# Kernel optimization log

Hardware: AMD Instinct MI355X
Metric: run time of the kernel (lower is better)

Reference implementation:

```python
import jax, jax.numpy as jnp
import numpy as np

N_NODES = 100000
N_EDGES = 1600000
D_IN = 128
LAYER_SIZES = [128, 128, 64]


def setup_inputs() -> dict:
    key = jax.random.key(0)
    ks = jax.random.split(key, 12)
    x = jax.random.normal(ks[0], (N_NODES, D_IN), dtype=jnp.float32)
    edge_index = jax.random.randint(ks[1], (2, N_EDGES), 0, N_NODES, dtype=jnp.int64)
    edge_weight = jax.random.uniform(ks[2], (N_EDGES,), dtype=jnp.float32)
    inp = {"x": x, "edge_index": edge_index, "edge_weight": edge_weight}
    dims = [D_IN] + LAYER_SIZES
    for i in range(len(LAYER_SIZES)):
        fan_in, fan_out = dims[i], dims[i + 1]
        # glorot-style init like PyG GCNConv
        scale = jnp.sqrt(6.0 / (fan_in + fan_out)).astype(jnp.float32)
        inp[f"W{i}"] = jax.random.uniform(ks[3 + 2 * i], (fan_in, fan_out), dtype=jnp.float32, minval=-scale, maxval=scale)
        inp[f"b{i}"] = jnp.zeros((fan_out,), dtype=jnp.float32)
    return inp


def _gcn_norm(edge_index, edge_weight, num_nodes):
    # PyG gcn_norm with add_self_loops=True (fill value 1.0)
    src, dst = edge_index[0], edge_index[1]
    loop = jnp.arange(num_nodes, dtype=edge_index.dtype)
    src_full = jnp.concatenate([src, loop])
    dst_full = jnp.concatenate([dst, loop])
    w_full = jnp.concatenate([edge_weight, jnp.ones((num_nodes,), dtype=edge_weight.dtype)])
    deg = jax.ops.segment_sum(w_full, dst_full, num_segments=num_nodes)  # [N]
    deg_inv_sqrt = jnp.where(deg > 0, jax.lax.rsqrt(jnp.where(deg > 0, deg, 1.0)), 0.0)
    norm = deg_inv_sqrt[src_full] * w_full * deg_inv_sqrt[dst_full]  # [E+N]
    return src_full, dst_full, norm


def _gcn_conv(x, src, dst, norm, W, b):
    h = x @ W                                  # [N, d_out] dense transform
    msg = h[src] * norm[:, None]               # [E+N, d_out] gather + scale
    out = jax.ops.segment_sum(msg, dst, num_segments=x.shape[0])  # scatter-add
    return out + b


def reference(x, edge_index, edge_weight, W0, b0, W1, b1, W2, b2):
    N = x.shape[0]
    src, dst, norm = _gcn_norm(edge_index, edge_weight, N)
    x = jax.nn.relu(_gcn_conv(x, src, dst, norm, W0, b0))
    x = jax.nn.relu(_gcn_conv(x, src, dst, norm, W1, b1))
    x = _gcn_conv(x, src, dst, norm, W2, b2)  # no ReLU on final layer
    return x
```

## Files before the change

### kernel.cpp

```cpp
#include <hip/hip_runtime.h>
#include <hip/hip_fp16.h>


typedef __attribute__((ext_vector_type(8))) _Float16 f16x8;
typedef __attribute__((ext_vector_type(4))) float f32x4;

#define WQ_BITS 15
#define WQ_SCALE 32768.0f
#define WQ_MASK 32767u

__global__ __launch_bounds__(256) void k_pre(int* cnt, int N,
                                             const float* __restrict__ W0,
                                             const float* __restrict__ W1,
                                             const float* __restrict__ W2,
                                             __half* __restrict__ wt0,
                                             __half* __restrict__ wt1,
                                             __half* __restrict__ wt2) {
    int id = blockIdx.x * 256 + threadIdx.x;
    if (id < N) cnt[id] = 0;
    if (id < 16384) {
        int n = id >> 7, k = id & 127;
        wt0[id] = __float2half(W0[k * 128 + n]);
    } else if (id < 32768) {
        int j = id - 16384, n = j >> 7, k = j & 127;
        wt1[j] = __float2half(W1[k * 128 + n]);
    } else if (id < 40960) {
        int j = id - 32768, n = j >> 7, k = j & 127;
        wt2[j] = __float2half(W2[k * 64 + n]);
    }
}

__global__ __launch_bounds__(256) void k_build(const int* __restrict__ src,
                                               const int* __restrict__ dst,
                                               const float* __restrict__ w,
                                               int* cnt, unsigned int* __restrict__ EW,
                                               int E, int cap) {
    const int p = blockIdx.x & 7;
    const int chunk = blockIdx.x >> 3;
    const int nchunk = gridDim.x >> 3;
    const int stride = nchunk * 256;
    for (int e = chunk * 256 + threadIdx.x; e < E; e += stride) {
        int t = dst[e];
        if (((t >> 4) & 7) != p) continue;
        int s = src[e];
        int wq = (int)(w[e] * WQ_SCALE + 0.5f);
        wq = (wq < (int)WQ_MASK) ? wq : (int)WQ_MASK;
        int k = atomicAdd(&cnt[t], 1);
        if (k < cap) EW[(size_t)t * cap + k] = ((unsigned int)s << WQ_BITS) | (unsigned int)wq;
    }
}

template <int BN, bool XFP32, bool DINV>
__global__ __launch_bounds__(256, 4) void k_gemm(const void* __restrict__ Xv,
                                                 const __half* __restrict__ Wt,
                                                 float* __restrict__ dinv,
                                                 const int* __restrict__ cnt,
                                                 const unsigned int* __restrict__ EW,
                                                 int cap,
                                                 __half* __restrict__ H, int N) {
    __shared__ float dinv_s[64];
    const int tid = threadIdx.x;
    const int lane = tid & 63;
    const int wv = tid >> 6;
    const int m = lane & 15;
    const int quad = lane >> 4;
    const int rb = blockIdx.x * 64;
    const int row = rb + wv * 16 + m;
    const int rowc = (row < N) ? row : (N - 1);

    if constexpr (DINV) {
        int rloc = tid >> 2, sub = tid & 3;
        int r = rb + rloc;
        float wsum = 0.f;
        if (r < N) {
            int c = cnt[r];
            c = (c < cap) ? c : cap;
            for (int j = sub; j < c; j += 4)
                wsum += (float)(EW[(size_t)r * cap + j] & WQ_MASK);
        }
        wsum += __shfl_xor(wsum, 1, 64);
        wsum += __shfl_xor(wsum, 2, 64);
        float dv = 1.0f / sqrtf(1.0f + wsum * (1.0f / WQ_SCALE));
        if (sub == 0) {
            dinv_s[rloc] = dv;
            if (r < N) dinv[r] = dv;
        }
        __syncthreads();
    }

    f16x8 xf[4];
    if constexpr (XFP32) {
        const float* X = (const float*)Xv;
#pragma unroll
        for (int s = 0; s < 4; s++) {
            const float4* p = (const float4*)(X + (size_t)rowc * 128 + s * 32 + quad * 8);
            float4 u0 = p[0], u1 = p[1];
            f16x8 f;
            f[0] = (_Float16)u0.x; f[1] = (_Float16)u0.y;
            f[2] = (_Float16)u0.z; f[3] = (_Float16)u0.w;
            f[4] = (_Float16)u1.x; f[5] = (_Float16)u1.y;
            f[6] = (_Float16)u1.z; f[7] = (_Float16)u1.w;
            xf[s] = f;
        }
    } else {
        const __half* X = (const __half*)Xv;
#pragma unroll
        for (int s = 0; s < 4; s++)
            xf[s] = *(const f16x8*)(X + (size_t)rowc * 128 + s * 32 + quad * 8);
    }

    constexpr int NT = BN / 16;
    f32x4 acc[NT];
#pragma unroll
    for (int t = 0; t < NT; t++) acc[t] = (f32x4){0.f, 0.f, 0.f, 0.f};

#pragma unroll
    for (int s = 0; s < 4; s++) {
#pragma unroll
        for (int t = 0; t < NT; t++) {
            f16x8 wf = *(const f16x8*)(Wt + (size_t)(t * 16 + m) * 128 + s * 32 + quad * 8);
            acc[t] = __builtin_amdgcn_mfma_f32_16x16x32_f16(wf, xf[s], acc[t], 0, 0, 0);
        }
    }

    if (row < N) {
        float sc = DINV ? dinv_s[wv * 16 + m] : dinv[row];
#pragma unroll
        for (int t = 0; t < NT; t++) {
            __half2 h0 = __floats2half2_rn(sc * acc[t][0], sc * acc[t][1]);
            __half2 h1 = __floats2half2_rn(sc * acc[t][2], sc * acc[t][3]);
            __half2* dstp = (__half2*)(H + (size_t)row * BN + t * 16 + quad * 4);
            dstp[0] = h0;
            dstp[1] = h1;
        }
    }
}

#define RL(v, k) __builtin_amdgcn_readlane((v), (k))

template <int DOUT, bool RELU>
__global__ __launch_bounds__(256) void k_agg(const __half* __restrict__ H,
                                             const unsigned int* __restrict__ EW,
                                             const int* __restrict__ cnt,
                                             const float* __restrict__ dinv,
                                             const float* __restrict__ bias,
                                             void* __restrict__ Outv,
                                             int N, int cap) {
    int node = blockIdx.x * 4 + (threadIdx.x >> 6);
    if (node >= N) return;
    const int lane = threadIdx.x & 63;

    int c = cnt[node];
    c = (c < cap) ? c : cap;

    unsigned int meta = 0;
    if (lane < c) meta = EW[(size_t)node * cap + lane];

    float dt = dinv[node];

    if constexpr (DOUT == 128) {
        const __half2* H2 = reinterpret_cast<const __half2*>(H);
        float2 hs = __half22float2(H2[(size_t)node * 64 + lane]);
        float a0 = hs.x, a1 = hs.y;
        int k = 0;
        for (; k + 8 <= c; k += 8) {
            __half2 hr[8]; float w[8];
#pragma unroll
            for (int u = 0; u < 8; u++) {
                unsigned int mm = RL(meta, k + u);
                w[u] = (float)(mm & WQ_MASK) * (1.0f / WQ_SCALE);
                hr[u] = H2[(size_t)(mm >> WQ_BITS) * 64 + lane];
            }
#pragma unroll
            for (int u = 0; u < 8; u++) {
                float2 hv = __half22float2(hr[u]);
                a0 = fmaf(w[u], hv.x, a0);
                a1 = fmaf(w[u], hv.y, a1);
            }
        }
        for (; k + 4 <= c; k += 4) {
            __half2 hr[4]; float w[4];
#pragma unroll
            for (int u = 0; u < 4; u++) {
                unsigned int mm = RL(meta, k + u);
                w[u] = (float)(mm & WQ_MASK) * (1.0f / WQ_SCALE);
                hr[u] = H2[(size_t)(mm >> WQ_BITS) * 64 + lane];
            }
#pragma unroll
            for (int u = 0; u < 4; u++) {
                float2 hv = __half22float2(hr[u]);
                a0 = fmaf(w[u], hv.x, a0);
                a1 = fmaf(w[u], hv.y, a1);
            }
        }
        for (; k < c; k++) {
            unsigned int mm = RL(meta, k);
            float w = (float)(mm & WQ_MASK) * (1.0f / WQ_SCALE);
            float2 hv = __half22float2(H2[(size_t)(mm >> WQ_BITS) * 64 + lane]);
            a0 = fmaf(w, hv.x, a0);
            a1 = fmaf(w, hv.y, a1);
        }
        float2 b = reinterpret_cast<const float2*>(bias)[lane];
        a0 = fmaf(dt, a0, b.x);
        a1 = fmaf(dt, a1, b.y);
        if (RELU) { a0 = fmaxf(a0, 0.f); a1 = fmaxf(a1, 0.f); }
        reinterpret_cast<__half2*>(Outv)[(size_t)node * 64 + lane] = __floats2half2_rn(a0, a1);
    } else {
        float a = __half2float(H[(size_t)node * 64 + lane]);
        int k = 0;
        for (; k + 8 <= c; k += 8) {
            __half hr[8]; float w[8];
#pragma unroll
            for (int u = 0; u < 8; u++) {
                unsigned int mm = RL(meta, k + u);
                w[u] = (float)(mm & WQ_MASK) * (1.0f / WQ_SCALE);
                hr[u] = H[(size_t)(mm >> WQ_BITS) * 64 + lane];
            }
#pragma unroll
            for (int u = 0; u < 8; u++) a = fmaf(w[u], __half2float(hr[u]), a);
        }
        for (; k < c; k++) {
            unsigned int mm = RL(meta, k);
            float w = (float)(mm & WQ_MASK) * (1.0f / WQ_SCALE);
            a = fmaf(w, __half2float(H[(size_t)(mm >> WQ_BITS) * 64 + lane]), a);
        }
        a = fmaf(dt, a, bias[lane]);
        if (RELU) a = fmaxf(a, 0.f);
        ((float*)Outv)[(size_t)node * 64 + lane] = a;
    }
}

extern "C" void kernel_launch(void* const* d_in, const int* in_sizes, int n_in,
                              void* d_out, int out_size, void* d_ws, size_t ws_size,
                              hipStream_t stream) {
    const int N = in_sizes[0] / 128;
    const int E = in_sizes[2];

    const float* x  = (const float*)d_in[0];
    const int*   ei = (const int*)d_in[1];
    const int*   src = ei;
    const int*   dst = ei + E;
    const float* ew  = (const float*)d_in[2];
    const float* W0 = (const float*)d_in[3];
    const float* b0 = (const float*)d_in[4];
    const float* W1 = (const float*)d_in[5];
    const float* b1 = (const float*)d_in[6];
    const float* W2 = (const float*)d_in[7];
    const float* b2 = (const float*)d_in[8];

    size_t fixed = (((size_t)N * 4 + 255) & ~(size_t)255)
                 + (((size_t)N * 4 + 255) & ~(size_t)255)
                 + 2 * (((size_t)N * 128 * 2 + 255) & ~(size_t)255)
                 + 3 * 33024
                 + 2048;
    int cap = 64;
    if (ws_size > fixed) {
        size_t avail = (ws_size - fixed) / ((size_t)N * 4);
        if (avail < (size_t)cap) cap = (int)avail;
    } else {
        cap = 0;
    }

    char* p = (char*)d_ws;
    auto alloc = [&](size_t bytes) -> void* {
        void* r = (void*)p;
        p += (bytes + 255) & ~(size_t)255;
        return r;
    };
    int*          cnt  = (int*)alloc((size_t)N * 4);
    float*        dinv = (float*)alloc((size_t)N * 4);
    unsigned int* EW   = (unsigned int*)alloc((size_t)N * cap * 4);
    __half*       bufH = (__half*)alloc((size_t)N * 128 * 2);
    __half*       bufA = (__half*)alloc((size_t)N * 128 * 2);
    __half*       wt0  = (__half*)alloc(16384 * 2);
    __half*       wt1  = (__half*)alloc(16384 * 2);
    __half*       wt2  = (__half*)alloc(8192 * 2);

    dim3 blk(256);
    int preN = (N > 40960) ? N : 40960;
    dim3 gPre((preN + 255) / 256);
    dim3 gBuild(6656);
    dim3 gGemm((N + 63) / 64);
    dim3 gWave((N + 3) / 4);

    k_pre<<<gPre, blk, 0, stream>>>(cnt, N, W0, W1, W2, wt0, wt1, wt2);
    k_build<<<gBuild, blk, 0, stream>>>(src, dst, ew, cnt, EW, E, cap);

    k_gemm<128, true, true><<<gGemm, blk, 0, stream>>>(x, wt0, dinv, cnt, EW, cap, bufH, N);
    k_agg<128, true><<<gWave, blk, 0, stream>>>(bufH, EW, cnt, dinv, b0, bufA, N, cap);

    k_gemm<128, false, false><<<gGemm, blk, 0, stream>>>(bufA, wt1, dinv, cnt, EW, cap, bufH, N);
    k_agg<128, true><<<gWave, blk, 0, stream>>>(bufH, EW, cnt, dinv, b1, bufA, N, cap);

    k_gemm<64, false, false><<<gGemm, blk, 0, stream>>>(bufA, wt2, dinv, cnt, EW, cap, bufH, N);
    k_agg<64, false><<<gWave, blk, 0, stream>>>(bufH, EW, cnt, dinv, b2,
                                                d_out, N, cap);
}
```

Baseline: 450.4 us.

## Build per-node edge lists via two-pass partition binning with LDS atomics

Replaces the single-pass global-atomic edge-list build, which scanned all edges eight times and did one global atomic per edge, with two kernels. The first bins edges into coarse node partitions using shared-memory histograms and one global atomic per block per partition. The second scatters each partition into per-node slots with LDS atomics and computes the degree normalisation there, so the first GEMM no longer recomputes it. This adds a 64-bit intermediate list stored in the H buffer and an extra launch, and edges past the per-partition capacity are dropped.

```diff
diff --git a/kernel.cpp b/kernel.cpp
--- a/kernel.cpp
+++ b/kernel.cpp
@@ -4,12 +4,16 @@
 
 typedef __attribute__((ext_vector_type(8))) _Float16 f16x8;
 typedef __attribute__((ext_vector_type(4))) float f32x4;
+typedef unsigned long long u64;
 
 #define WQ_BITS 15
 #define WQ_SCALE 32768.0f
 #define WQ_MASK 32767u
-
-__global__ __launch_bounds__(256) void k_pre(int* cnt, int N,
+#define MAXNP 2048
+
+#define RL(v, k) __builtin_amdgcn_readlane((v), (k))
+
+__global__ __launch_bounds__(256) void k_pre(int* tail, int NP,
                                              const float* __restrict__ W0,
                                              const float* __restrict__ W1,
                                              const float* __restrict__ W2,
@@ -17,7 +21,7 @@
                                              __half* __restrict__ wt1,
                                              __half* __restrict__ wt2) {
     int id = blockIdx.x * 256 + threadIdx.x;
-    if (id < N) cnt[id] = 0;
+    if (id < NP) tail[id] = 0;
     if (id < 16384) {
         int n = id >> 7, k = id & 127;
         wt0[id] = __float2half(W0[k * 128 + n]);
@@ -30,35 +34,88 @@
     }
 }
 
-__global__ __launch_bounds__(256) void k_build(const int* __restrict__ src,
-                                               const int* __restrict__ dst,
-                                               const float* __restrict__ w,
-                                               int* cnt, unsigned int* __restrict__ EW,
-                                               int E, int cap) {
-    const int p = blockIdx.x & 7;
-    const int chunk = blockIdx.x >> 3;
-    const int nchunk = gridDim.x >> 3;
-    const int stride = nchunk * 256;
-    for (int e = chunk * 256 + threadIdx.x; e < E; e += stride) {
+__global__ __launch_bounds__(256) void k_bin(const int* __restrict__ src,
+                                             const int* __restrict__ dst,
+                                             const float* __restrict__ w,
+                                             int* tail, u64* __restrict__ glist,
+                                             int E, int ecap, int NP, int shift) {
+    __shared__ unsigned int h[MAXNP];
+    __shared__ int base[MAXNP];
+    const int nb = gridDim.x;
+    const int per = (E + nb - 1) / nb;
+    const int e0 = blockIdx.x * per;
+    const int e1 = (e0 + per < E) ? e0 + per : E;
+
+    for (int i = threadIdx.x; i < NP; i += 256) h[i] = 0;
+    __syncthreads();
+    for (int e = e0 + (int)threadIdx.x; e < e1; e += 256) {
+        int p = dst[e] >> shift;
+        atomicAdd(&h[p], 1u);
+    }
+    __syncthreads();
+    for (int i = threadIdx.x; i < NP; i += 256) {
+        unsigned int c = h[i];
+        base[i] = c ? atomicAdd(&tail[i], (int)c) : 0;
+    }
+    __syncthreads();
+    for (int e = e0 + (int)threadIdx.x; e < e1; e += 256) {
         int t = dst[e];
-        if (((t >> 4) & 7) != p) continue;
-        int s = src[e];
-        int wq = (int)(w[e] * WQ_SCALE + 0.5f);
+        int p = t >> shift;
+        int s = __builtin_nontemporal_load(src + e);
+        float we = __builtin_nontemporal_load(w + e);
+        int wq = (int)(we * WQ_SCALE + 0.5f);
         wq = (wq < (int)WQ_MASK) ? wq : (int)WQ_MASK;
-        int k = atomicAdd(&cnt[t], 1);
-        if (k < cap) EW[(size_t)t * cap + k] = ((unsigned int)s << WQ_BITS) | (unsigned int)wq;
-    }
-}
-
-template <int BN, bool XFP32, bool DINV>
+        u64 v = ((u64)(unsigned)t << 32) |
+                ((unsigned)s << WQ_BITS) | (unsigned)wq;
+        unsigned int idx = atomicSub(&h[p], 1u) - 1u;
+        int pos = base[p] + (int)idx;
+        if (pos < ecap) glist[(size_t)p * ecap + pos] = v;
+    }
+}
+
+__global__ __launch_bounds__(256) void k_fill(const int* __restrict__ tail,
+                                              const u64* __restrict__ glist,
+                                              int ecap, int* __restrict__ cnt,
+                                              float* __restrict__ dinv,
+                                              unsigned int* __restrict__ EW,
+                                              int cap, int N, int shift) {
+    __shared__ unsigned int lcnt[MAXNP];
+    __shared__ float lws[MAXNP];
+    const int p = blockIdx.x;
+    const int np = 1 << shift;
+    const int t0 = p << shift;
+    for (int i = threadIdx.x; i < np; i += 256) { lcnt[i] = 0; lws[i] = 0.f; }
+    __syncthreads();
+    int n = tail[p];
+    if (n > ecap) n = ecap;
+    const u64* L = glist + (size_t)p * ecap;
+    for (int j = threadIdx.x; j < n; j += 256) {
+        u64 v = L[j];
+        int t = (int)(v >> 32);
+        int loc = t - t0;
+        unsigned int k = atomicAdd(&lcnt[loc], 1u);
+        if ((int)k < cap) {
+            EW[(size_t)t * cap + k] = (unsigned int)v;
+            atomicAdd(&lws[loc], (float)((unsigned int)v & WQ_MASK));
+        }
+    }
+    __syncthreads();
+    for (int i = threadIdx.x; i < np; i += 256) {
+        int t = t0 + i;
+        if (t < N) {
+            int c = (int)lcnt[i];
+            c = (c < cap) ? c : cap;
+            cnt[t] = c;
+            dinv[t] = 1.0f / sqrtf(1.0f + lws[i] * (1.0f / WQ_SCALE));
+        }
+    }
+}
+
+template <int BN, bool XFP32>
 __global__ __launch_bounds__(256, 4) void k_gemm(const void* __restrict__ Xv,
                                                  const __half* __restrict__ Wt,
-                                                 float* __restrict__ dinv,
-                                                 const int* __restrict__ cnt,
-                                                 const unsigned int* __restrict__ EW,
-                                                 int cap,
+                                                 const float* __restrict__ dinv,
                                                  __half* __restrict__ H, int N) {
-    __shared__ float dinv_s[64];
     const int tid = threadIdx.x;
     const int lane = tid & 63;
     const int wv = tid >> 6;
@@ -67,26 +124,6 @@
     const int rb = blockIdx.x * 64;
     const int row = rb + wv * 16 + m;
     const int rowc = (row < N) ? row : (N - 1);
-
-    if constexpr (DINV) {
-        int rloc = tid >> 2, sub = tid & 3;
-        int r = rb + rloc;
-        float wsum = 0.f;
-        if (r < N) {
-            int c = cnt[r];
-            c = (c < cap) ? c : cap;
-            for (int j = sub; j < c; j += 4)
-                wsum += (float)(EW[(size_t)r * cap + j] & WQ_MASK);
-        }
-        wsum += __shfl_xor(wsum, 1, 64);
-        wsum += __shfl_xor(wsum, 2, 64);
-        float dv = 1.0f / sqrtf(1.0f + wsum * (1.0f / WQ_SCALE));
-        if (sub == 0) {
-            dinv_s[rloc] = dv;
-            if (r < N) dinv[r] = dv;
-        }
-        __syncthreads();
-    }
 
     f16x8 xf[4];
     if constexpr (XFP32) {
@@ -124,7 +161,7 @@
     }
 
     if (row < N) {
-        float sc = DINV ? dinv_s[wv * 16 + m] : dinv[row];
+        float sc = dinv[row];
 #pragma unroll
         for (int t = 0; t < NT; t++) {
             __half2 h0 = __floats2half2_rn(sc * acc[t][0], sc * acc[t][1]);
@@ -135,8 +172,6 @@
         }
     }
 }
-
-#define RL(v, k) __builtin_amdgcn_readlane((v), (k))
 
 template <int DOUT, bool RELU>
 __global__ __launch_bounds__(256) void k_agg(const __half* __restrict__ H,
@@ -248,10 +283,15 @@
     const float* W2 = (const float*)d_in[7];
     const float* b2 = (const float*)d_in[8];
 
+    int shift = 6;
+    while ((((N - 1) >> shift) + 1) > MAXNP) shift++;
+    const int NP = ((N - 1) >> shift) + 1;
+
     size_t fixed = (((size_t)N * 4 + 255) & ~(size_t)255)
                  + (((size_t)N * 4 + 255) & ~(size_t)255)
                  + 2 * (((size_t)N * 128 * 2 + 255) & ~(size_t)255)
                  + 3 * 33024
+                 + (((size_t)NP * 4 + 255) & ~(size_t)255)
                  + 2048;
     int cap = 64;
     if (ws_size > fixed) {
@@ -275,24 +315,30 @@
     __half*       wt0  = (__half*)alloc(16384 * 2);
     __half*       wt1  = (__half*)alloc(16384 * 2);
     __half*       wt2  = (__half*)alloc(8192 * 2);
+    int*          tail = (int*)alloc((size_t)NP * 4);
+
+    u64* glist = (u64*)bufH;
+    int  ecap  = (int)(((size_t)N * 128 * 2) / ((size_t)NP * 8));
 
     dim3 blk(256);
-    int preN = (N > 40960) ? N : 40960;
+    int preN = (NP > 40960) ? NP : 40960;
     dim3 gPre((preN + 255) / 256);
-    dim3 gBuild(6656);
+    dim3 gBin(256);
+    dim3 gFill(NP);
     dim3 gGemm((N + 63) / 64);
     dim3 gWave((N + 3) / 4);
 
-    k_pre<<<gPre, blk, 0, stream>>>(cnt, N, W0, W1, W2, wt0, wt1, wt2);
-    k_build<<<gBuild, blk, 0, stream>>>(src, dst, ew, cnt, EW, E, cap);
-
-    k_gemm<128, true, true><<<gGemm, blk, 0, stream>>>(x, wt0, dinv, cnt, EW, cap, bufH, N);
+    k_pre<<<gPre, blk, 0, stream>>>(tail, NP, W0, W1, W2, wt0, wt1, wt2);
+    k_bin<<<gBin, blk, 0, stream>>>(src, dst, ew, tail, glist, E, ecap, NP, shift);
+    k_fill<<<gFill, blk, 0, stream>>>(tail, glist, ecap, cnt, dinv, EW, cap, N, shift);
+
+    k_gemm<128, true><<<gGemm, blk, 0, stream>>>(x, wt0, dinv, bufH, N);
     k_agg<128, true><<<gWave, blk, 0, stream>>>(bufH, EW, cnt, dinv, b0, bufA, N, cap);
 
-    k_gemm<128, false, false><<<gGemm, blk, 0, stream>>>(bufA, wt1, dinv, cnt, EW, cap, bufH, N);
+    k_gemm<128, false><<<gGemm, blk, 0, stream>>>(bufA, wt1, dinv, bufH, N);
     k_agg<128, true><<<gWave, blk, 0, stream>>>(bufH, EW, cnt, dinv, b1, bufA, N, cap);
 
-    k_gemm<64, false, false><<<gGemm, blk, 0, stream>>>(bufA, wt2, dinv, cnt, EW, cap, bufH, N);
+    k_gemm<64, false><<<gGemm, blk, 0, stream>>>(bufA, wt2, dinv, bufH, N);
     k_agg<64, false><<<gWave, blk, 0, stream>>>(bufH, EW, cnt, dinv, b2,
                                                 d_out, N, cap);
 }
```

After: 435.7 us. -3.3%, faster.
